# Kernel optimization log

Hardware: AMD Instinct MI355X
Metric: run time of the kernel (lower is better)

Reference implementation:

```python
import jax, jax.numpy as jnp
import numpy as np

# Sizes: N news nodes, E 'similar' edges, 768-d input, hidden 64, 4 heads, 2 HGT layers, 2 classes
N, E, F_IN, HID, H, L, C = 100000, 1600000, 768, 64, 4, 2, 2
D = HID // H  # per-head dim = 16


def setup_inputs() -> dict:
    key = jax.random.key(0)
    ks = jax.random.split(key, 16)
    s = 0.05
    nrm = lambda k, shape: jax.random.normal(k, shape, jnp.float32) * s
    return {
        "x": jax.random.normal(ks[0], (N, F_IN), jnp.float32),
        "edge_index": jax.random.randint(ks[1], (2, E), 0, N, jnp.int32),
        # input projection
        "Wp": nrm(ks[2], (F_IN, HID)), "bp": jnp.zeros((HID,), jnp.float32),
        # per-layer HGT params (stacked over L layers)
        "Wk": nrm(ks[3], (L, HID, HID)), "bk": jnp.zeros((L, HID), jnp.float32),
        "Wq": nrm(ks[4], (L, HID, HID)), "bq": jnp.zeros((L, HID), jnp.float32),
        "Wv": nrm(ks[5], (L, HID, HID)), "bv": jnp.zeros((L, HID), jnp.float32),
        "a_rel": nrm(ks[6], (L, H, D, D)),  # per-edge-type attention transform
        "m_rel": nrm(ks[7], (L, H, D, D)),  # per-edge-type message transform
        "p_rel": jnp.ones((L, H), jnp.float32),  # relation prior
        "Wo": nrm(ks[8], (L, HID, HID)), "bo": jnp.zeros((L, HID), jnp.float32),
        "skip": jnp.ones((L,), jnp.float32),
        # classifier MLP: 64 -> 32 -> 2
        "Wc1": nrm(ks[9], (HID, HID // 2)), "bc1": jnp.zeros((HID // 2,), jnp.float32),
        "Wc2": nrm(ks[10], (HID // 2, C)), "bc2": jnp.zeros((C,), jnp.float32),
    }


def _hgt_layer(h, src, dst, Wk, bk, Wq, bq, Wv, bv, a_rel, m_rel, p_rel, Wo, bo, skip):
    n = h.shape[0]
    k = (h @ Wk + bk).reshape(n, H, D)
    q = (h @ Wq + bq).reshape(n, H, D)
    v = (h @ Wv + bv).reshape(n, H, D)
    # per-edge attention logits: (k_src @ a_rel) . q_dst * p_rel / sqrt(D)
    k_e = jnp.einsum('ehd,hdf->ehf', k[src], a_rel)          # [E,H,D]
    alpha = jnp.einsum('ehf,ehf->eh', k_e, q[dst]) * p_rel / np.float32(np.sqrt(D))
    # segment softmax over incoming edges of each dst node
    mx = jax.ops.segment_max(alpha, dst, num_segments=n)     # [N,H]
    a = jnp.exp(alpha - mx[dst])
    denom = jax.ops.segment_sum(a, dst, num_segments=n)
    a = a / (denom[dst] + 1e-16)
    # messages + scatter-add aggregation
    msg = jnp.einsum('ehd,hdf->ehf', v[src], m_rel)          # [E,H,D]
    agg = jax.ops.segment_sum(a[..., None] * msg, dst, num_segments=n).reshape(n, HID)
    out = jax.nn.gelu(agg) @ Wo + bo
    g = jax.nn.sigmoid(skip)
    return g * out + (1.0 - g) * h  # skip connection (same dims)


def reference(x, edge_index, Wp, bp, Wk, bk, Wq, bq, Wv, bv, a_rel, m_rel, p_rel,
              Wo, bo, skip, Wc1, bc1, Wc2, bc2):
    src, dst = edge_index[0], edge_index[1]
    h = x @ Wp + bp
    for l in range(L):
        h = _hgt_layer(h, src, dst, Wk[l], bk[l], Wq[l], bq[l], Wv[l], bv[l],
                       a_rel[l], m_rel[l], p_rel[l], Wo[l], bo[l], skip[l])
        h = jax.nn.relu(h)  # dropout is identity in eval mode
    hc = jax.nn.relu(h @ Wc1 + bc1)
    return hc @ Wc2 + bc2  # [N, C] logits
```

## Files before the change

kernel.cpp:

```cpp
#include <hip/hip_runtime.h>
#include <math.h>


typedef __attribute__((ext_vector_type(8))) short bf16x8;
typedef __attribute__((ext_vector_type(4))) float f32x4;

__device__ __forceinline__ float gelu_t(float x) {
  const float c = 0.7978845608028654f;
  float t = tanhf(c * (x + 0.044715f * x * x * x));
  return 0.5f * x * (1.0f + t);
}

__device__ __forceinline__ void split1(float a, ushort& h, ushort& l) {
  unsigned u = __float_as_uint(a);
  unsigned uh = u & 0xffff0000u;
  float fl = a - __uint_as_float(uh);
  h = (ushort)(uh >> 16);
  l = (ushort)(__float_as_uint(fl) >> 16);
}

template<int CTRL>
__device__ __forceinline__ float row_ror_add(float v) {
  int r = __builtin_amdgcn_update_dpp(0, __float_as_int(v), CTRL, 0xF, 0xF, true);
  return v + __int_as_float(r);
}
__device__ __forceinline__ float red16(float v) {
  v = row_ror_add<0x121>(v);
  v = row_ror_add<0x122>(v);
  v = row_ror_add<0x124>(v);
  v = row_ror_add<0x128>(v);
  return v;
}

template<int K, bool PRE_GELU, bool EPI_SKIP>
__global__ __launch_bounds__(256, 4)
void mfma_gemm(const float* __restrict__ A, int ldA,
               const ushort* __restrict__ Wt,
               const float* __restrict__ bias,
               const float* __restrict__ Hprev,
               const float* __restrict__ skipPtr,
               float* __restrict__ outp, int ldOut, int nRows)
{
  constexpr int NCH = K / 32;
  __shared__ ushort sA[2 * 64 * 32];
  __shared__ ushort sB[2 * 64 * 32];
  const int tid = threadIdx.x;
  const int lane = tid & 63;
  const int wv = tid >> 6;
  const int m = lane & 15;
  const int q = lane >> 4;
  const int row0 = blockIdx.x * 64;
  const int colBlk = blockIdx.y * 64;

  const int srow = tid >> 2;
  const int skoff = (tid & 3) * 8;
  int gr = row0 + srow; if (gr >= nRows) gr = nRows - 1;
  const float* aBase = A + (size_t)gr * ldA + skoff;
  const float4* wBase = (const float4*)(Wt + (size_t)blockIdx.y * NCH * 4096);

  f32x4 acc[4];
#pragma unroll
  for (int ct = 0; ct < 4; ++ct) acc[ct] = (f32x4){0.f, 0.f, 0.f, 0.f};

  float4 a0 = *(const float4*)(aBase + 0);
  float4 a1 = *(const float4*)(aBase + 4);
  float4 b0 = wBase[tid * 2];
  float4 b1 = wBase[tid * 2 + 1];

#pragma clang loop unroll(disable)
  for (int ch = 0; ch < NCH; ++ch) {
    float4 na0 = a0, na1 = a1, nb0 = b0, nb1 = b1;
    if (ch + 1 < NCH) {
      na0 = *(const float4*)(aBase + (ch + 1) * 32);
      na1 = *(const float4*)(aBase + (ch + 1) * 32 + 4);
      const float4* wc = wBase + (size_t)(ch + 1) * 512;
      nb0 = wc[tid * 2];
      nb1 = wc[tid * 2 + 1];
    }
    float av[8] = {a0.x, a0.y, a0.z, a0.w, a1.x, a1.y, a1.z, a1.w};
    if (PRE_GELU) {
#pragma unroll
      for (int j = 0; j < 8; ++j) av[j] = gelu_t(av[j]);
    }
    bf16x8 vh, vl;
#pragma unroll
    for (int j = 0; j < 8; ++j) {
      ushort h, l; split1(av[j], h, l);
      vh[j] = (short)h; vl[j] = (short)l;
    }
    __syncthreads();
    *(bf16x8*)(sA + srow * 32 + skoff) = vh;
    *(bf16x8*)(sA + 2048 + srow * 32 + skoff) = vl;
    ((float4*)sB)[tid * 2] = b0;
    ((float4*)sB)[tid * 2 + 1] = b1;
    __syncthreads();
    bf16x8 ah = *(const bf16x8*)(sA + (wv * 16 + m) * 32 + q * 8);
    bf16x8 al = *(const bf16x8*)(sA + 2048 + (wv * 16 + m) * 32 + q * 8);
#pragma unroll
    for (int ct = 0; ct < 4; ++ct) {
      bf16x8 bh = *(const bf16x8*)(sB + (ct * 16 + m) * 32 + q * 8);
      bf16x8 bl = *(const bf16x8*)(sB + 2048 + (ct * 16 + m) * 32 + q * 8);
      acc[ct] = __builtin_amdgcn_mfma_f32_16x16x32_bf16(ah, bh, acc[ct], 0, 0, 0);
      acc[ct] = __builtin_amdgcn_mfma_f32_16x16x32_bf16(ah, bl, acc[ct], 0, 0, 0);
      acc[ct] = __builtin_amdgcn_mfma_f32_16x16x32_bf16(al, bh, acc[ct], 0, 0, 0);
    }
    a0 = na0; a1 = na1; b0 = nb0; b1 = nb1;
  }

  float g = 0.f, gi = 0.f;
  if (EPI_SKIP) { g = 1.0f / (1.0f + __expf(-skipPtr[0])); gi = 1.0f - g; }
#pragma unroll
  for (int ct = 0; ct < 4; ++ct) {
    int c = colBlk + ct * 16 + m;
    float b = bias[c];
#pragma unroll
    for (int i = 0; i < 4; ++i) {
      int r = row0 + wv * 16 + q * 4 + i;
      if (r < nRows) {
        float o = acc[ct][i] + b;
        if (EPI_SKIP) {
          float hp = Hprev[(size_t)r * 64 + c];
          o = fmaxf(g * o + gi * hp, 0.f);
        }
        outp[(size_t)r * ldOut + c] = o;
      }
    }
  }
}

template<int CB, bool PRE_GELU, bool EPI_SKIP>
__global__ __launch_bounds__(256, 2)
void mfma_gemm_k64(const float* __restrict__ A,
                   const ushort* __restrict__ Wt,
                   const float* __restrict__ bias,
                   const float* __restrict__ Hprev,
                   const float* __restrict__ skipPtr,
                   float* __restrict__ outp, int ldOut, int nRows)
{
  __shared__ ushort sA[2 * 4096];
  __shared__ ushort sB[CB][2 * 4096];
  const int tid = threadIdx.x;
  const int lane = tid & 63;
  const int wv = tid >> 6;
  const int m = lane & 15;
  const int q = lane >> 4;
  const int row0 = blockIdx.x * 64;
  const int srow = tid >> 2;
  const int skoff = (tid & 3) * 8;
  int gr = row0 + srow; if (gr >= nRows) gr = nRows - 1;
  const float* aBase = A + (size_t)gr * 64 + skoff;
  const float4* wBase = (const float4*)Wt;

  float4 a0 = *(const float4*)(aBase + 0);
  float4 a1 = *(const float4*)(aBase + 4);
  float4 a2 = *(const float4*)(aBase + 32);
  float4 a3 = *(const float4*)(aBase + 36);
  float4 bb0[CB], bb1[CB], bb2[CB], bb3[CB];
#pragma unroll
  for (int cb = 0; cb < CB; ++cb) {
    bb0[cb] = wBase[(size_t)(cb * 2 + 0) * 512 + tid * 2];
    bb1[cb] = wBase[(size_t)(cb * 2 + 0) * 512 + tid * 2 + 1];
    bb2[cb] = wBase[(size_t)(cb * 2 + 1) * 512 + tid * 2];
    bb3[cb] = wBase[(size_t)(cb * 2 + 1) * 512 + tid * 2 + 1];
  }

  {
    float av[16] = {a0.x, a0.y, a0.z, a0.w, a1.x, a1.y, a1.z, a1.w,
                    a2.x, a2.y, a2.z, a2.w, a3.x, a3.y, a3.z, a3.w};
    if (PRE_GELU) {
#pragma unroll
      for (int j = 0; j < 16; ++j) av[j] = gelu_t(av[j]);
    }
    bf16x8 vh0, vl0, vh1, vl1;
#pragma unroll
    for (int j = 0; j < 8; ++j) {
      ushort h, l; split1(av[j], h, l);
      vh0[j] = (short)h; vl0[j] = (short)l;
    }
#pragma unroll
    for (int j = 0; j < 8; ++j) {
      ushort h, l; split1(av[8 + j], h, l);
      vh1[j] = (short)h; vl1[j] = (short)l;
    }
    *(bf16x8*)(sA + srow * 32 + skoff) = vh0;
    *(bf16x8*)(sA + 2048 + srow * 32 + skoff) = vl0;
    *(bf16x8*)(sA + 4096 + srow * 32 + skoff) = vh1;
    *(bf16x8*)(sA + 4096 + 2048 + srow * 32 + skoff) = vl1;
  }
#pragma unroll
  for (int cb = 0; cb < CB; ++cb) {
    ((float4*)(sB[cb]))[tid * 2] = bb0[cb];
    ((float4*)(sB[cb]))[tid * 2 + 1] = bb1[cb];
    ((float4*)(sB[cb] + 4096))[tid * 2] = bb2[cb];
    ((float4*)(sB[cb] + 4096))[tid * 2 + 1] = bb3[cb];
  }
  __syncthreads();

  f32x4 acc[CB][4];
#pragma unroll
  for (int cb = 0; cb < CB; ++cb)
#pragma unroll
    for (int ct = 0; ct < 4; ++ct) acc[cb][ct] = (f32x4){0.f, 0.f, 0.f, 0.f};

  bf16x8 ah0 = *(const bf16x8*)(sA + (wv * 16 + m) * 32 + q * 8);
  bf16x8 al0 = *(const bf16x8*)(sA + 2048 + (wv * 16 + m) * 32 + q * 8);
  bf16x8 ah1 = *(const bf16x8*)(sA + 4096 + (wv * 16 + m) * 32 + q * 8);
  bf16x8 al1 = *(const bf16x8*)(sA + 4096 + 2048 + (wv * 16 + m) * 32 + q * 8);
#pragma unroll
  for (int cb = 0; cb < CB; ++cb) {
#pragma unroll
    for (int ct = 0; ct < 4; ++ct) {
      bf16x8 bh0 = *(const bf16x8*)(sB[cb] + (ct * 16 + m) * 32 + q * 8);
      bf16x8 bl0 = *(const bf16x8*)(sB[cb] + 2048 + (ct * 16 + m) * 32 + q * 8);
      acc[cb][ct] = __builtin_amdgcn_mfma_f32_16x16x32_bf16(ah0, bh0, acc[cb][ct], 0, 0, 0);
      acc[cb][ct] = __builtin_amdgcn_mfma_f32_16x16x32_bf16(ah0, bl0, acc[cb][ct], 0, 0, 0);
      acc[cb][ct] = __builtin_amdgcn_mfma_f32_16x16x32_bf16(al0, bh0, acc[cb][ct], 0, 0, 0);
      bf16x8 bh1 = *(const bf16x8*)(sB[cb] + 4096 + (ct * 16 + m) * 32 + q * 8);
      bf16x8 bl1 = *(const bf16x8*)(sB[cb] + 4096 + 2048 + (ct * 16 + m) * 32 + q * 8);
      acc[cb][ct] = __builtin_amdgcn_mfma_f32_16x16x32_bf16(ah1, bh1, acc[cb][ct], 0, 0, 0);
      acc[cb][ct] = __builtin_amdgcn_mfma_f32_16x16x32_bf16(ah1, bl1, acc[cb][ct], 0, 0, 0);
      acc[cb][ct] = __builtin_amdgcn_mfma_f32_16x16x32_bf16(al1, bh1, acc[cb][ct], 0, 0, 0);
    }
  }

  float g = 0.f, gi = 0.f;
  if (EPI_SKIP) { g = 1.0f / (1.0f + __expf(-skipPtr[0])); gi = 1.0f - g; }
#pragma unroll
  for (int cb = 0; cb < CB; ++cb) {
#pragma unroll
    for (int ct = 0; ct < 4; ++ct) {
      int c = cb * 64 + ct * 16 + m;
      float b = bias[c];
#pragma unroll
      for (int i = 0; i < 4; ++i) {
        int r = row0 + wv * 16 + q * 4 + i;
        if (r < nRows) {
          float o = acc[cb][ct][i] + b;
          if (EPI_SKIP) {
            float hp = Hprev[(size_t)r * 64 + c];
            o = fmaxf(g * o + gi * hp, 0.f);
          }
          outp[(size_t)r * ldOut + c] = o;
        }
      }
    }
  }
}

__global__ void prep_weights(const float* __restrict__ W, int K, int C,
                             ushort* __restrict__ Wt)
{
  int idx = blockIdx.x * 256 + threadIdx.x;
  if (idx < K * C) {
    int k = idx / C, c = idx % C;
    ushort h, l; split1(W[idx], h, l);
    int cb = c >> 6, cc = c & 63, ch = k >> 5, kk = k & 31;
    size_t base = (size_t)(cb * (K >> 5) + ch) * 4096;
    Wt[base + cc * 32 + kk] = h;
    Wt[base + 2048 + cc * 32 + kk] = l;
  }
}

__global__ void fold_weights(const float* __restrict__ Wq, const float* __restrict__ bq,
                             const float* __restrict__ Wk, const float* __restrict__ bk,
                             const float* __restrict__ Wv, const float* __restrict__ bv,
                             const float* __restrict__ a_rel, const float* __restrict__ m_rel,
                             float* __restrict__ Wqkv, float* __restrict__ bqkv)
{
  int l = blockIdx.x;
  const float* wq = Wq + l * 4096; const float* wk = Wk + l * 4096; const float* wv = Wv + l * 4096;
  const float* bql = bq + l * 64;  const float* bkl = bk + l * 64;  const float* bvl = bv + l * 64;
  const float* ar = a_rel + l * 1024; const float* mr = m_rel + l * 1024;
  float* W = Wqkv + l * 64 * 192;  float* B = bqkv + l * 192;
  for (int t = threadIdx.x; t < 64 * 192; t += blockDim.x) {
    int i = t / 192, c = t % 192;
    float val;
    int cp;
    if (c < 64) {
      val = wq[i * 64 + c];
      cp = c;
    } else if (c < 128) {
      int cc = c - 64, hh = cc >> 4, f = cc & 15;
      float s = 0.f;
      for (int d = 0; d < 16; ++d) s += wk[i * 64 + hh * 16 + d] * ar[hh * 256 + d * 16 + f];
      val = s;
      cp = 64 + (cc << 1);
    } else {
      int cc = c - 128, hh = cc >> 4, f = cc & 15;
      float s = 0.f;
      for (int d = 0; d < 16; ++d) s += wv[i * 64 + hh * 16 + d] * mr[hh * 256 + d * 16 + f];
      val = s;
      cp = 64 + (cc << 1) + 1;
    }
    W[i * 192 + cp] = val;
  }
  for (int c = threadIdx.x; c < 192; c += blockDim.x) {
    float val;
    int cp;
    if (c < 64) {
      val = bql[c];
      cp = c;
    } else if (c < 128) {
      int cc = c - 64, hh = cc >> 4, f = cc & 15;
      float s = 0.f;
      for (int d = 0; d < 16; ++d) s += bkl[hh * 16 + d] * ar[hh * 256 + d * 16 + f];
      val = s;
      cp = 64 + (cc << 1);
    } else {
      int cc = c - 128, hh = cc >> 4, f = cc & 15;
      float s = 0.f;
      for (int d = 0; d < 16; ++d) s += bvl[hh * 16 + d] * mr[hh * 256 + d * 16 + f];
      val = s;
      cp = 64 + (cc << 1) + 1;
    }
    B[cp] = val;
  }
}

__global__ void hist_kernel(const int* __restrict__ dst, int* __restrict__ counts, int E) {
  int e = blockIdx.x * 256 + threadIdx.x;
  if (e < E) atomicAdd(&counts[dst[e]], 1);
}

__global__ __launch_bounds__(256)
void scanA(int* __restrict__ counts, int* __restrict__ blockSums, int n) {
  __shared__ int sd[256];
  int tid = threadIdx.x;
  int base = blockIdx.x * 1024 + tid * 4;
  int v[4];
#pragma unroll
  for (int j = 0; j < 4; ++j) v[j] = (base + j < n) ? counts[base + j] : 0;
  int t = v[0] + v[1] + v[2] + v[3];
  sd[tid] = t; __syncthreads();
  for (int offm = 1; offm < 256; offm <<= 1) {
    int adj = (tid >= offm) ? sd[tid - offm] : 0;
    __syncthreads();
    sd[tid] += adj;
    __syncthreads();
  }
  int run = sd[tid] - t;
#pragma unroll
  for (int j = 0; j < 4; ++j) {
    if (base + j < n) counts[base + j] = run;
    run += v[j];
  }
  if (tid == 255) blockSums[blockIdx.x] = sd[255];
}

__global__ void scanB(int* __restrict__ blockSums, int G, int* __restrict__ row_ptr, int n) {
  __shared__ int sd[128];
  int tid = threadIdx.x;
  int t = (tid < G) ? blockSums[tid] : 0;
  sd[tid] = t; __syncthreads();
  for (int offm = 1; offm < 128; offm <<= 1) {
    int adj = (tid >= offm) ? sd[tid - offm] : 0;
    __syncthreads();
    sd[tid] += adj;
    __syncthreads();
  }
  if (tid < G) blockSums[tid] = sd[tid] - t;
  if (tid == 127) row_ptr[n] = sd[127];
}

__global__ void scanC(const int* __restrict__ counts, const int* __restrict__ blockSums,
                      int* __restrict__ row_ptr, int* __restrict__ cursor, int n) {
  int idx = blockIdx.x * 256 + threadIdx.x;
  if (idx < n) {
    int v = counts[idx] + blockSums[idx >> 10];
    row_ptr[idx] = v;
    cursor[idx] = v;
  }
}

__global__ void scatter_kernel(const int* __restrict__ src, const int* __restrict__ dst,
                               int* __restrict__ cursor, int* __restrict__ csr_src, int E) {
  int e = blockIdx.x * 256 + threadIdx.x;
  if (e < E) {
    int d = dst[e];
    int pos = atomicAdd(&cursor[d], 1);
    csr_src[pos] = src[e];
  }
}

__global__ __launch_bounds__(256)
void edge_agg(const float* __restrict__ qkv, const int* __restrict__ row_ptr,
              const int* __restrict__ csr_src, const float* __restrict__ p_rel,
              float* __restrict__ agg, int n)
{
  int wid = blockIdx.x * 4 + (threadIdx.x >> 6);
  if (wid >= n) return;
  int lane = threadIdx.x & 63;
  int head = lane >> 4;
  float pr = p_rel[head] * 0.25f;
  float qv = qkv[(size_t)wid * 192 + lane] * pr;
  int e0 = __builtin_amdgcn_readfirstlane(row_ptr[wid]);
  int e1 = __builtin_amdgcn_readfirstlane(row_ptr[wid + 1]);
  const float* ktb = qkv + 64 + 2 * lane;
  float num = 0.f, den = 0.f;
  for (int e = e0; e < e1; e += 8) {
    int last = e1 - 1;
    int i1 = (e + 1 < e1) ? e + 1 : last;
    int i2 = (e + 2 < e1) ? e + 2 : last;
    int i3 = (e + 3 < e1) ? e + 3 : last;
    int i4 = (e + 4 < e1) ? e + 4 : last;
    int i5 = (e + 5 < e1) ? e + 5 : last;
    int i6 = (e + 6 < e1) ? e + 6 : last;
    int i7 = (e + 7 < e1) ? e + 7 : last;
    int s0 = __builtin_amdgcn_readfirstlane(csr_src[e]);
    int s1 = __builtin_amdgcn_readfirstlane(csr_src[i1]);
    int s2 = __builtin_amdgcn_readfirstlane(csr_src[i2]);
    int s3 = __builtin_amdgcn_readfirstlane(csr_src[i3]);
    int s4 = __builtin_amdgcn_readfirstlane(csr_src[i4]);
    int s5 = __builtin_amdgcn_readfirstlane(csr_src[i5]);
    int s6 = __builtin_amdgcn_readfirstlane(csr_src[i6]);
    int s7 = __builtin_amdgcn_readfirstlane(csr_src[i7]);
    float2 kv0 = *(const float2*)(ktb + (size_t)s0 * 192);
    float2 kv1 = *(const float2*)(ktb + (size_t)s1 * 192);
    float2 kv2 = *(const float2*)(ktb + (size_t)s2 * 192);
    float2 kv3 = *(const float2*)(ktb + (size_t)s3 * 192);
    float2 kv4 = *(const float2*)(ktb + (size_t)s4 * 192);
    float2 kv5 = *(const float2*)(ktb + (size_t)s5 * 192);
    float2 kv6 = *(const float2*)(ktb + (size_t)s6 * 192);
    float2 kv7 = *(const float2*)(ktb + (size_t)s7 * 192);
    float p0 = red16(kv0.x * qv);
    float p1 = red16(kv1.x * qv);
    float p2 = red16(kv2.x * qv);
    float p3 = red16(kv3.x * qv);
    float p4 = red16(kv4.x * qv);
    float p5 = red16(kv5.x * qv);
    float p6 = red16(kv6.x * qv);
    float p7 = red16(kv7.x * qv);
    float w0 = __expf(p0);
    float w1 = (e + 1 < e1) ? __expf(p1) : 0.f;
    float w2 = (e + 2 < e1) ? __expf(p2) : 0.f;
    float w3 = (e + 3 < e1) ? __expf(p3) : 0.f;
    float w4 = (e + 4 < e1) ? __expf(p4) : 0.f;
    float w5 = (e + 5 < e1) ? __expf(p5) : 0.f;
    float w6 = (e + 6 < e1) ? __expf(p6) : 0.f;
    float w7 = (e + 7 < e1) ? __expf(p7) : 0.f;
    den += ((w0 + w1) + (w2 + w3)) + ((w4 + w5) + (w6 + w7));
    num = fmaf(w0, kv0.y, num);
    num = fmaf(w1, kv1.y, num);
    num = fmaf(w2, kv2.y, num);
    num = fmaf(w3, kv3.y, num);
    num = fmaf(w4, kv4.y, num);
    num = fmaf(w5, kv5.y, num);
    num = fmaf(w6, kv6.y, num);
    num = fmaf(w7, kv7.y, num);
  }
  agg[(size_t)wid * 64 + lane] = num / (den + 1e-16f);
}

__global__ __launch_bounds__(256)
void classifier(const float* __restrict__ h, const float* __restrict__ Wc1,
                const float* __restrict__ bc1, const float* __restrict__ Wc2,
                const float* __restrict__ bc2, float* __restrict__ out, int n)
{
  int row = blockIdx.x * 256 + threadIdx.x;
  if (row >= n) return;
  float hid[32];
#pragma unroll
  for (int j = 0; j < 32; ++j) hid[j] = bc1[j];
  const float* hr = h + (size_t)row * 64;
#pragma unroll 4
  for (int k = 0; k < 64; k += 4) {
    float4 x = *(const float4*)&hr[k];
#pragma unroll
    for (int j = 0; j < 32; ++j) {
      hid[j] += x.x * Wc1[k * 32 + j] + x.y * Wc1[(k + 1) * 32 + j]
              + x.z * Wc1[(k + 2) * 32 + j] + x.w * Wc1[(k + 3) * 32 + j];
    }
  }
  float o0 = bc2[0], o1 = bc2[1];
#pragma unroll
  for (int j = 0; j < 32; ++j) {
    float v = fmaxf(hid[j], 0.f);
    o0 += v * Wc2[j * 2 + 0];
    o1 += v * Wc2[j * 2 + 1];
  }
  *(float2*)&out[(size_t)row * 2] = make_float2(o0, o1);
}

extern "C" void kernel_launch(void* const* d_in, const int* in_sizes, int n_in,
                              void* d_out, int out_size, void* d_ws, size_t ws_size,
                              hipStream_t stream)
{
  const float* x     = (const float*)d_in[0];
  const int*  eidx   = (const int*)d_in[1];
  const float* Wp    = (const float*)d_in[2];
  const float* bp    = (const float*)d_in[3];
  const float* Wk    = (const float*)d_in[4];
  const float* bk    = (const float*)d_in[5];
  const float* Wq    = (const float*)d_in[6];
  const float* bq    = (const float*)d_in[7];
  const float* Wv    = (const float*)d_in[8];
  const float* bv    = (const float*)d_in[9];
  const float* a_rel = (const float*)d_in[10];
  const float* m_rel = (const float*)d_in[11];
  const float* p_rel = (const float*)d_in[12];
  const float* Wo    = (const float*)d_in[13];
  const float* bo    = (const float*)d_in[14];
  const float* skip  = (const float*)d_in[15];
  const float* Wc1   = (const float*)d_in[16];
  const float* bc1   = (const float*)d_in[17];
  const float* Wc2   = (const float*)d_in[18];
  const float* bc2   = (const float*)d_in[19];
  float* out = (float*)d_out;

  const int N = in_sizes[0] / 768;
  const int E = in_sizes[1] / 2;
  const int* srcIdx = eidx;
  const int* dstIdx = eidx + E;

  char* ws = (char*)d_ws;
  size_t off = 0;
  auto alloc = [&](size_t bytes) -> void* {
    void* p = ws + off;
    off = (off + bytes + 255) & ~(size_t)255;
    return p;
  };
  float* h     = (float*)alloc((size_t)N * 64 * 4);
  float* qkv   = (float*)alloc((size_t)N * 192 * 4);
  float* agg   = (float*)alloc((size_t)N * 64 * 4);
  float* Wqkv  = (float*)alloc(2 * 64 * 192 * 4);
  float* bqkv  = (float*)alloc(2 * 192 * 4);
  int* row_ptr = (int*)alloc((size_t)(N + 1) * 4);
  int* cursor  = (int*)alloc((size_t)N * 4);
  int* counts  = (int*)alloc((size_t)N * 4);
  int* blockSums = (int*)alloc(512 * 4);
  int* csr_src = (int*)alloc((size_t)E * 4);
  ushort* WtP   = (ushort*)alloc((size_t)64 * 768 * 2 * 2);
  ushort* WtQKV = (ushort*)alloc((size_t)2 * 192 * 64 * 2 * 2);
  ushort* WtO   = (ushort*)alloc((size_t)2 * 64 * 64 * 2 * 2);
  (void)ws_size; (void)n_in; (void)out_size;

  hipMemsetAsync(counts, 0, (size_t)N * 4, stream);

  fold_weights<<<2, 256, 0, stream>>>(Wq, bq, Wk, bk, Wv, bv, a_rel, m_rel, Wqkv, bqkv);

  prep_weights<<<(768 * 64 + 255) / 256, 256, 0, stream>>>(Wp, 768, 64, WtP);
  for (int l = 0; l < 2; ++l) {
    prep_weights<<<(64 * 192 + 255) / 256, 256, 0, stream>>>(
        Wqkv + l * 64 * 192, 64, 192, WtQKV + (size_t)l * 192 * 64 * 2);
    prep_weights<<<(64 * 64 + 255) / 256, 256, 0, stream>>>(
        Wo + l * 4096, 64, 64, WtO + (size_t)l * 64 * 64 * 2);
  }

  mfma_gemm<768, false, false><<<dim3((N + 63) / 64, 1), 256, 0, stream>>>(
      x, 768, WtP, bp, nullptr, nullptr, h, 64, N);

  hist_kernel<<<(E + 255) / 256, 256, 0, stream>>>(dstIdx, counts, E);
  int G = (N + 1023) / 1024;
  scanA<<<G, 256, 0, stream>>>(counts, blockSums, N);
  scanB<<<1, 128, 0, stream>>>(blockSums, G, row_ptr, N);
  scanC<<<(N + 255) / 256, 256, 0, stream>>>(counts, blockSums, row_ptr, cursor, N);
  scatter_kernel<<<(E + 255) / 256, 256, 0, stream>>>(srcIdx, dstIdx, cursor, csr_src, E);

  for (int l = 0; l < 2; ++l) {
    mfma_gemm_k64<3, false, false><<<(N + 63) / 64, 256, 0, stream>>>(
        h, WtQKV + (size_t)l * 192 * 64 * 2, bqkv + l * 192,
        nullptr, nullptr, qkv, 192, N);
    edge_agg<<<(N + 3) / 4, 256, 0, stream>>>(qkv, row_ptr, csr_src, p_rel + l * 4, agg, N);
    mfma_gemm_k64<1, true, true><<<(N + 63) / 64, 256, 0, stream>>>(
        agg, WtO + (size_t)l * 64 * 64 * 2, bo + l * 64, h, skip + l, h, 64, N);
  }

  classifier<<<(N + 255) / 256, 256, 0, stream>>>(h, Wc1, bc1, Wc2, bc2, out, N);
}
```

Before: 1.071 ms.

## Store folded K/V as packed fp16 pairs to halve edge gather traffic

The QKV GEMM epilogue now writes Q in fp32 and the folded K and V values as interleaved half2 pairs, shrinking each node row from 192 floats to 128 float-sized slots. The edge aggregation kernel gathers one half2 per lane per edge instead of a float2, cutting the random-gather bytes that dominate this kernel. The interleaving moves from the fold_weights column permutation into the GEMM epilogue, and the projection GEMM loses its unused template paths. The k64 GEMM with a single column block now requests higher occupancy. Storing K and V in fp16 lowers their precision, and the csr_src readfirstlane calls are dropped.

```diff
diff --git a/kernel.cpp b/kernel.cpp
--- a/kernel.cpp
+++ b/kernel.cpp
@@ -1,4 +1,5 @@
 #include <hip/hip_runtime.h>
+#include <hip/hip_fp16.h>
 #include <math.h>
 
 
@@ -32,13 +33,11 @@
   return v;
 }
 
-template<int K, bool PRE_GELU, bool EPI_SKIP>
+template<int K>
 __global__ __launch_bounds__(256, 4)
 void mfma_gemm(const float* __restrict__ A, int ldA,
                const ushort* __restrict__ Wt,
                const float* __restrict__ bias,
-               const float* __restrict__ Hprev,
-               const float* __restrict__ skipPtr,
                float* __restrict__ outp, int ldOut, int nRows)
 {
   constexpr int NCH = K / 32;
@@ -78,10 +77,6 @@
       nb1 = wc[tid * 2 + 1];
     }
     float av[8] = {a0.x, a0.y, a0.z, a0.w, a1.x, a1.y, a1.z, a1.w};
-    if (PRE_GELU) {
-#pragma unroll
-      for (int j = 0; j < 8; ++j) av[j] = gelu_t(av[j]);
-    }
     bf16x8 vh, vl;
 #pragma unroll
     for (int j = 0; j < 8; ++j) {
@@ -107,8 +102,6 @@
     a0 = na0; a1 = na1; b0 = nb0; b1 = nb1;
   }
 
-  float g = 0.f, gi = 0.f;
-  if (EPI_SKIP) { g = 1.0f / (1.0f + __expf(-skipPtr[0])); gi = 1.0f - g; }
 #pragma unroll
   for (int ct = 0; ct < 4; ++ct) {
     int c = colBlk + ct * 16 + m;
@@ -116,20 +109,13 @@
 #pragma unroll
     for (int i = 0; i < 4; ++i) {
       int r = row0 + wv * 16 + q * 4 + i;
-      if (r < nRows) {
-        float o = acc[ct][i] + b;
-        if (EPI_SKIP) {
-          float hp = Hprev[(size_t)r * 64 + c];
-          o = fmaxf(g * o + gi * hp, 0.f);
-        }
-        outp[(size_t)r * ldOut + c] = o;
-      }
-    }
-  }
-}
-
-template<int CB, bool PRE_GELU, bool EPI_SKIP>
-__global__ __launch_bounds__(256, 2)
+      if (r < nRows) outp[(size_t)r * ldOut + c] = acc[ct][i] + b;
+    }
+  }
+}
+
+template<int CB, int EPI>
+__global__ __launch_bounds__(256, (CB == 1) ? 4 : 2)
 void mfma_gemm_k64(const float* __restrict__ A,
                    const ushort* __restrict__ Wt,
                    const float* __restrict__ bias,
@@ -167,7 +153,7 @@
   {
     float av[16] = {a0.x, a0.y, a0.z, a0.w, a1.x, a1.y, a1.z, a1.w,
                     a2.x, a2.y, a2.z, a2.w, a3.x, a3.y, a3.z, a3.w};
-    if (PRE_GELU) {
+    if (EPI == 1) {
 #pragma unroll
       for (int j = 0; j < 16; ++j) av[j] = gelu_t(av[j]);
     }
@@ -223,24 +209,41 @@
     }
   }
 
-  float g = 0.f, gi = 0.f;
-  if (EPI_SKIP) { g = 1.0f / (1.0f + __expf(-skipPtr[0])); gi = 1.0f - g; }
-#pragma unroll
-  for (int cb = 0; cb < CB; ++cb) {
+  if (EPI == 2) {
 #pragma unroll
     for (int ct = 0; ct < 4; ++ct) {
-      int c = cb * 64 + ct * 16 + m;
-      float b = bias[c];
+      int c = ct * 16 + m;
+      float bq_ = bias[c], bk_ = bias[64 + c], bv_ = bias[128 + c];
 #pragma unroll
       for (int i = 0; i < 4; ++i) {
         int r = row0 + wv * 16 + q * 4 + i;
         if (r < nRows) {
-          float o = acc[cb][ct][i] + b;
-          if (EPI_SKIP) {
-            float hp = Hprev[(size_t)r * 64 + c];
-            o = fmaxf(g * o + gi * hp, 0.f);
+          outp[(size_t)r * 128 + c] = acc[0][ct][i] + bq_;
+          __half2 kv = __floats2half2_rn(acc[1][ct][i] + bk_, acc[2][ct][i] + bv_);
+          *((__half2*)outp + (size_t)r * 128 + 64 + c) = kv;
+        }
+      }
+    }
+  } else {
+    float g = 0.f, gi = 0.f;
+    if (EPI == 1) { g = 1.0f / (1.0f + __expf(-skipPtr[0])); gi = 1.0f - g; }
+#pragma unroll
+    for (int cb = 0; cb < CB; ++cb) {
+#pragma unroll
+      for (int ct = 0; ct < 4; ++ct) {
+        int c = cb * 64 + ct * 16 + m;
+        float b = bias[c];
+#pragma unroll
+        for (int i = 0; i < 4; ++i) {
+          int r = row0 + wv * 16 + q * 4 + i;
+          if (r < nRows) {
+            float o = acc[cb][ct][i] + b;
+            if (EPI == 1) {
+              float hp = Hprev[(size_t)r * 64 + c];
+              o = fmaxf(g * o + gi * hp, 0.f);
+            }
+            outp[(size_t)r * ldOut + c] = o;
           }
-          outp[(size_t)r * ldOut + c] = o;
         }
       }
     }
@@ -275,45 +278,37 @@
   for (int t = threadIdx.x; t < 64 * 192; t += blockDim.x) {
     int i = t / 192, c = t % 192;
     float val;
-    int cp;
     if (c < 64) {
       val = wq[i * 64 + c];
-      cp = c;
     } else if (c < 128) {
       int cc = c - 64, hh = cc >> 4, f = cc & 15;
       float s = 0.f;
       for (int d = 0; d < 16; ++d) s += wk[i * 64 + hh * 16 + d] * ar[hh * 256 + d * 16 + f];
       val = s;
-      cp = 64 + (cc << 1);
     } else {
       int cc = c - 128, hh = cc >> 4, f = cc & 15;
       float s = 0.f;
       for (int d = 0; d < 16; ++d) s += wv[i * 64 + hh * 16 + d] * mr[hh * 256 + d * 16 + f];
       val = s;
-      cp = 64 + (cc << 1) + 1;
-    }
-    W[i * 192 + cp] = val;
+    }
+    W[i * 192 + c] = val;
   }
   for (int c = threadIdx.x; c < 192; c += blockDim.x) {
     float val;
-    int cp;
     if (c < 64) {
       val = bql[c];
-      cp = c;
     } else if (c < 128) {
       int cc = c - 64, hh = cc >> 4, f = cc & 15;
       float s = 0.f;
       for (int d = 0; d < 16; ++d) s += bkl[hh * 16 + d] * ar[hh * 256 + d * 16 + f];
       val = s;
-      cp = 64 + (cc << 1);
     } else {
       int cc = c - 128, hh = cc >> 4, f = cc & 15;
       float s = 0.f;
       for (int d = 0; d < 16; ++d) s += bvl[hh * 16 + d] * mr[hh * 256 + d * 16 + f];
       val = s;
-      cp = 64 + (cc << 1) + 1;
-    }
-    B[cp] = val;
+    }
+    B[c] = val;
   }
 }
 
@@ -392,10 +387,10 @@
   int lane = threadIdx.x & 63;
   int head = lane >> 4;
   float pr = p_rel[head] * 0.25f;
-  float qv = qkv[(size_t)wid * 192 + lane] * pr;
+  float qv = qkv[(size_t)wid * 128 + lane] * pr;
   int e0 = __builtin_amdgcn_readfirstlane(row_ptr[wid]);
   int e1 = __builtin_amdgcn_readfirstlane(row_ptr[wid + 1]);
-  const float* ktb = qkv + 64 + 2 * lane;
+  const __half2* ktb = (const __half2*)qkv + 64 + lane;
   float num = 0.f, den = 0.f;
   for (int e = e0; e < e1; e += 8) {
     int last = e1 - 1;
@@ -406,30 +401,30 @@
     int i5 = (e + 5 < e1) ? e + 5 : last;
     int i6 = (e + 6 < e1) ? e + 6 : last;
     int i7 = (e + 7 < e1) ? e + 7 : last;
-    int s0 = __builtin_amdgcn_readfirstlane(csr_src[e]);
-    int s1 = __builtin_amdgcn_readfirstlane(csr_src[i1]);
-    int s2 = __builtin_amdgcn_readfirstlane(csr_src[i2]);
-    int s3 = __builtin_amdgcn_readfirstlane(csr_src[i3]);
-    int s4 = __builtin_amdgcn_readfirstlane(csr_src[i4]);
-    int s5 = __builtin_amdgcn_readfirstlane(csr_src[i5]);
-    int s6 = __builtin_amdgcn_readfirstlane(csr_src[i6]);
-    int s7 = __builtin_amdgcn_readfirstlane(csr_src[i7]);
-    float2 kv0 = *(const float2*)(ktb + (size_t)s0 * 192);
-    float2 kv1 = *(const float2*)(ktb + (size_t)s1 * 192);
-    float2 kv2 = *(const float2*)(ktb + (size_t)s2 * 192);
-    float2 kv3 = *(const float2*)(ktb + (size_t)s3 * 192);
-    float2 kv4 = *(const float2*)(ktb + (size_t)s4 * 192);
-    float2 kv5 = *(const float2*)(ktb + (size_t)s5 * 192);
-    float2 kv6 = *(const float2*)(ktb + (size_t)s6 * 192);
-    float2 kv7 = *(const float2*)(ktb + (size_t)s7 * 192);
-    float p0 = red16(kv0.x * qv);
-    float p1 = red16(kv1.x * qv);
-    float p2 = red16(kv2.x * qv);
-    float p3 = red16(kv3.x * qv);
-    float p4 = red16(kv4.x * qv);
-    float p5 = red16(kv5.x * qv);
-    float p6 = red16(kv6.x * qv);
-    float p7 = red16(kv7.x * qv);
+    int s0 = csr_src[e];
+    int s1 = csr_src[i1];
+    int s2 = csr_src[i2];
+    int s3 = csr_src[i3];
+    int s4 = csr_src[i4];
+    int s5 = csr_src[i5];
+    int s6 = csr_src[i6];
+    int s7 = csr_src[i7];
+    float2 f0 = __half22float2(ktb[(size_t)s0 * 128]);
+    float2 f1 = __half22float2(ktb[(size_t)s1 * 128]);
+    float2 f2 = __half22float2(ktb[(size_t)s2 * 128]);
+    float2 f3 = __half22float2(ktb[(size_t)s3 * 128]);
+    float2 f4 = __half22float2(ktb[(size_t)s4 * 128]);
+    float2 f5 = __half22float2(ktb[(size_t)s5 * 128]);
+    float2 f6 = __half22float2(ktb[(size_t)s6 * 128]);
+    float2 f7 = __half22float2(ktb[(size_t)s7 * 128]);
+    float p0 = red16(f0.x * qv);
+    float p1 = red16(f1.x * qv);
+    float p2 = red16(f2.x * qv);
+    float p3 = red16(f3.x * qv);
+    float p4 = red16(f4.x * qv);
+    float p5 = red16(f5.x * qv);
+    float p6 = red16(f6.x * qv);
+    float p7 = red16(f7.x * qv);
     float w0 = __expf(p0);
     float w1 = (e + 1 < e1) ? __expf(p1) : 0.f;
     float w2 = (e + 2 < e1) ? __expf(p2) : 0.f;
@@ -439,14 +434,14 @@
     float w6 = (e + 6 < e1) ? __expf(p6) : 0.f;
     float w7 = (e + 7 < e1) ? __expf(p7) : 0.f;
     den += ((w0 + w1) + (w2 + w3)) + ((w4 + w5) + (w6 + w7));
-    num = fmaf(w0, kv0.y, num);
-    num = fmaf(w1, kv1.y, num);
-    num = fmaf(w2, kv2.y, num);
-    num = fmaf(w3, kv3.y, num);
-    num = fmaf(w4, kv4.y, num);
-    num = fmaf(w5, kv5.y, num);
-    num = fmaf(w6, kv6.y, num);
-    num = fmaf(w7, kv7.y, num);
+    num = fmaf(w0, f0.y, num);
+    num = fmaf(w1, f1.y, num);
+    num = fmaf(w2, f2.y, num);
+    num = fmaf(w3, f3.y, num);
+    num = fmaf(w4, f4.y, num);
+    num = fmaf(w5, f5.y, num);
+    num = fmaf(w6, f6.y, num);
+    num = fmaf(w7, f7.y, num);
   }
   agg[(size_t)wid * 64 + lane] = num / (den + 1e-16f);
 }
@@ -520,7 +515,7 @@
     return p;
   };
   float* h     = (float*)alloc((size_t)N * 64 * 4);
-  float* qkv   = (float*)alloc((size_t)N * 192 * 4);
+  float* qkv   = (float*)alloc((size_t)N * 128 * 4);
   float* agg   = (float*)alloc((size_t)N * 64 * 4);
   float* Wqkv  = (float*)alloc(2 * 64 * 192 * 4);
   float* bqkv  = (float*)alloc(2 * 192 * 4);
@@ -546,8 +541,8 @@
         Wo + l * 4096, 64, 64, WtO + (size_t)l * 64 * 64 * 2);
   }
 
-  mfma_gemm<768, false, false><<<dim3((N + 63) / 64, 1), 256, 0, stream>>>(
-      x, 768, WtP, bp, nullptr, nullptr, h, 64, N);
+  mfma_gemm<768><<<dim3((N + 63) / 64, 1), 256, 0, stream>>>(
+      x, 768, WtP, bp, h, 64, N);
 
   hist_kernel<<<(E + 255) / 256, 256, 0, stream>>>(dstIdx, counts, E);
   int G = (N + 1023) / 1024;
@@ -557,11 +552,11 @@
   scatter_kernel<<<(E + 255) / 256, 256, 0, stream>>>(srcIdx, dstIdx, cursor, csr_src, E);
 
   for (int l = 0; l < 2; ++l) {
-    mfma_gemm_k64<3, false, false><<<(N + 63) / 64, 256, 0, stream>>>(
+    mfma_gemm_k64<3, 2><<<(N + 63) / 64, 256, 0, stream>>>(
         h, WtQKV + (size_t)l * 192 * 64 * 2, bqkv + l * 192,
-        nullptr, nullptr, qkv, 192, N);
+        nullptr, nullptr, qkv, 128, N);
     edge_agg<<<(N + 3) / 4, 256, 0, stream>>>(qkv, row_ptr, csr_src, p_rel + l * 4, agg, N);
-    mfma_gemm_k64<1, true, true><<<(N + 63) / 64, 256, 0, stream>>>(
+    mfma_gemm_k64<1, 1><<<(N + 63) / 64, 256, 0, stream>>>(
         agg, WtO + (size_t)l * 64 * 64 * 2, bo + l * 64, h, skip + l, h, 64, N);
   }
 
```

Result: faster. 937.9 us (-12.4%).
